# Performance work log

Hardware: AMD Instinct MI355X
Metric: run time of the kernel (lower is better)

Reference implementation:

```python
import jax, jax.numpy as jnp
import numpy as np

T, B, I, H = 2048, 512, 1, 64


def setup_inputs() -> dict:
    key = jax.random.key(0)
    ks = jax.random.split(key, 8)
    s_in = 1.0 / np.sqrt(H)  # torch RNN/Linear init scale (uniform bound)
    return {
        "x": jax.random.normal(ks[0], (T, B, I), dtype=jnp.float32),
        "h": jax.random.normal(ks[1], (1, B, H), dtype=jnp.float32),
        "W_ih": jax.random.uniform(ks[2], (H, I), jnp.float32, -s_in, s_in),
        "W_hh": jax.random.uniform(ks[3], (H, H), jnp.float32, -s_in, s_in),
        "b_ih": jax.random.uniform(ks[4], (H,), jnp.float32, -s_in, s_in),
        "b_hh": jax.random.uniform(ks[5], (H,), jnp.float32, -s_in, s_in),
        "W_lin": jax.random.uniform(ks[6], (1, H), jnp.float32, -s_in, s_in),
        "b_lin": jax.random.uniform(ks[7], (1,), jnp.float32, -s_in, s_in),
    }


def reference(x, h, W_ih, W_hh, b_ih, b_hh, W_lin, b_lin):
    # tanh RNN: h_t = tanh(x_t W_ih^T + b_ih + h_{t-1} W_hh^T + b_hh)
    h0 = h[0]  # [B, H]
    # precompute input projection for all timesteps: [T, B, H]
    xp = jnp.einsum('tbi,hi->tbh', x, W_ih) + b_ih + b_hh

    def step(h_prev, xp_t):
        h_new = jnp.tanh(xp_t + h_prev @ W_hh.T)
        return h_new, h_new

    h_last, hs = jax.lax.scan(step, h0, xp)  # hs: [T, B, H]
    y = jnp.einsum('tbh,oh->tbo', hs, W_lin) + b_lin  # [T, B, 1]
    return y, h_last[None]  # h_n: [1, B, H]
```

## Files before the change

kernel.cpp:

```cpp
#include <hip/hip_runtime.h>

#define TT 2048
#define BB 512
#define HH 64
#define NW 4
#define NTH (NW * 64)
#define HIST 128
#define HPAD 68

typedef float f32x2 __attribute__((ext_vector_type(2)));
typedef float f32x4 __attribute__((ext_vector_type(4)));

#define DPP_ADD(v, ctrl) \
    ((v) + __int_as_float(__builtin_amdgcn_update_dpp(0, __float_as_int(v), (ctrl), 0xF, 0xF, false)))

__global__ __launch_bounds__(NTH, 1) void rnn_fused(
    const float* __restrict__ x,
    const float* __restrict__ h0,
    const float* __restrict__ Wih,
    const float* __restrict__ Whh,
    const float* __restrict__ bih,
    const float* __restrict__ bhh,
    const float* __restrict__ Wlin,
    const float* __restrict__ blin,
    float* __restrict__ y,
    float* __restrict__ hN)
{
    __shared__ __align__(16) float hist[HIST][HPAD];
    __shared__ float xsh[TT + 4];
    __shared__ __align__(16) float wlin_sh[HH];

    const int b    = blockIdx.x;
    const int tid  = threadIdx.x;
    const int lane = tid & 63;
    const int w    = tid >> 6;
    const int hl   = lane >> 2;
    const int ks   = lane & 3;
    const int h    = w * 16 + hl;

    for (int i = tid; i < TT; i += NTH)
        xsh[i] = x[(size_t)i * BB + b];
    if (tid < 4) xsh[TT + tid] = 0.f;

    f32x2 wr[8];
    const float* wp = Whh + h * HH + ks * 16;
#pragma unroll
    for (int i = 0; i < 8; ++i) {
        wr[i][0] = wp[2 * i + 0];
        wr[i][1] = wp[2 * i + 1];
    }
    const float wih  = Wih[h];
    const float bias = bih[h] + bhh[h];
    const float bl   = blin[0];

    if (tid < HH) {
        hist[HIST - 1][tid] = h0[b * HH + tid];
        wlin_sh[tid] = Wlin[tid];
    }
    __syncthreads();

    float hval = 0.f;
    float xw = fmaf(xsh[0], wih, bias);

#pragma unroll 1
    for (int tc = 0; tc < TT; tc += HIST) {
#pragma unroll 2
        for (int ti = 0; ti < HIST; ++ti) {
            const int t  = tc + ti;
            const int rs = (ti + HIST - 1) & (HIST - 1);

            const f32x4* hp = reinterpret_cast<const f32x4*>(&hist[rs][ks * 16]);
            const f32x4 q0 = hp[0], q1 = hp[1], q2 = hp[2], q3 = hp[3];

            f32x2 a01 = {0.f, 0.f}, a23 = {0.f, 0.f};
            f32x2 a45 = {0.f, 0.f}, a67 = {0.f, 0.f};
            a01 = __builtin_elementwise_fma(__builtin_shufflevector(q0, q0, 0, 1), wr[0], a01);
            a23 = __builtin_elementwise_fma(__builtin_shufflevector(q0, q0, 2, 3), wr[1], a23);
            a45 = __builtin_elementwise_fma(__builtin_shufflevector(q1, q1, 0, 1), wr[2], a45);
            a67 = __builtin_elementwise_fma(__builtin_shufflevector(q1, q1, 2, 3), wr[3], a67);
            a01 = __builtin_elementwise_fma(__builtin_shufflevector(q2, q2, 0, 1), wr[4], a01);
            a23 = __builtin_elementwise_fma(__builtin_shufflevector(q2, q2, 2, 3), wr[5], a23);
            a45 = __builtin_elementwise_fma(__builtin_shufflevector(q3, q3, 0, 1), wr[6], a45);
            a67 = __builtin_elementwise_fma(__builtin_shufflevector(q3, q3, 2, 3), wr[7], a67);
            const f32x2 s2 = (a01 + a23) + (a45 + a67);
            float s = s2[0] + s2[1];

            s = DPP_ADD(s, 0xB1);
            s = DPP_ADD(s, 0x4E);

            const float acc = xw + s;

            const float e2 = __builtin_amdgcn_exp2f(acc * 2.885390081777927f);
            const float r  = __builtin_amdgcn_rcpf(e2 + 1.0f);
            hval = fmaf(-2.0f, r, 1.0f);

            if (ks == 0) hist[ti][h] = hval;

            xw = fmaf(xsh[t + 1], wih, bias);

            __syncthreads();
        }

        if (tid < HIST) {
            const f32x4* hp = reinterpret_cast<const f32x4*>(&hist[tid][0]);
            const f32x4* wl = reinterpret_cast<const f32x4*>(&wlin_sh[0]);
            f32x2 acc2 = {0.f, 0.f};
#pragma unroll
            for (int i = 0; i < 16; ++i) {
                const f32x4 q  = hp[i];
                const f32x4 qw = wl[i];
                acc2 = __builtin_elementwise_fma(__builtin_shufflevector(q, q, 0, 1),
                                                 __builtin_shufflevector(qw, qw, 0, 1), acc2);
                acc2 = __builtin_elementwise_fma(__builtin_shufflevector(q, q, 2, 3),
                                                 __builtin_shufflevector(qw, qw, 2, 3), acc2);
            }
            y[(size_t)(tc + tid) * BB + b] = acc2[0] + acc2[1] + bl;
        }
        __syncthreads();
    }

    if (ks == 0) hN[b * HH + h] = hval;
}

extern "C" void kernel_launch(void* const* d_in, const int* in_sizes, int n_in,
                              void* d_out, int out_size, void* d_ws, size_t ws_size,
                              hipStream_t stream) {
    const float* x    = (const float*)d_in[0];
    const float* h0   = (const float*)d_in[1];
    const float* Wih  = (const float*)d_in[2];
    const float* Whh  = (const float*)d_in[3];
    const float* bih  = (const float*)d_in[4];
    const float* bhh  = (const float*)d_in[5];
    const float* Wlin = (const float*)d_in[6];
    const float* blin = (const float*)d_in[7];

    float* y  = (float*)d_out;
    float* hN = (float*)d_out + TT * BB;

    rnn_fused<<<dim3(BB), dim3(NTH), 0, stream>>>(x, h0, Wih, Whh, bih, bhh, Wlin, blin, y, hN);
}
```

Before: 425.3 us.

## Use one wavefront per batch row with full-row dot, dropping block barriers

Each block now runs a single 64-lane wavefront. Every lane owns one hidden unit and computes the full 64-element dot product from 64 register-held weights, so the 4-way split with its DPP reduction and the per-timestep __syncthreads go away. The cost is four times more FMAs and LDS reads per lane on the serial critical path. Correctness without barriers depends on wavefront lockstep ordering of LDS writes and reads, which is fragile.

```diff
diff --git a/kernel.cpp b/kernel.cpp
--- a/kernel.cpp
+++ b/kernel.cpp
@@ -3,18 +3,17 @@
 #define TT 2048
 #define BB 512
 #define HH 64
-#define NW 4
-#define NTH (NW * 64)
 #define HIST 128
 #define HPAD 68
 
 typedef float f32x2 __attribute__((ext_vector_type(2)));
 typedef float f32x4 __attribute__((ext_vector_type(4)));
 
-#define DPP_ADD(v, ctrl) \
-    ((v) + __int_as_float(__builtin_amdgcn_update_dpp(0, __float_as_int(v), (ctrl), 0xF, 0xF, false)))
+#define FMA2(a, b, c) __builtin_elementwise_fma((a), (b), (c))
+#define LO2(q) __builtin_shufflevector((q), (q), 0, 1)
+#define HI2(q) __builtin_shufflevector((q), (q), 2, 3)
 
-__global__ __launch_bounds__(NTH, 1) void rnn_fused(
+__global__ __launch_bounds__(64, 1) void rnn_fused(
     const float* __restrict__ x,
     const float* __restrict__ h0,
     const float* __restrict__ Wih,
@@ -30,22 +29,17 @@
     __shared__ float xsh[TT + 4];
     __shared__ __align__(16) float wlin_sh[HH];
 
-    const int b    = blockIdx.x;
-    const int tid  = threadIdx.x;
-    const int lane = tid & 63;
-    const int w    = tid >> 6;
-    const int hl   = lane >> 2;
-    const int ks   = lane & 3;
-    const int h    = w * 16 + hl;
+    const int b = blockIdx.x;
+    const int h = threadIdx.x;
 
-    for (int i = tid; i < TT; i += NTH)
+    for (int i = h; i < TT; i += 64)
         xsh[i] = x[(size_t)i * BB + b];
-    if (tid < 4) xsh[TT + tid] = 0.f;
+    if (h < 4) xsh[TT + h] = 0.f;
 
-    f32x2 wr[8];
-    const float* wp = Whh + h * HH + ks * 16;
+    f32x2 wr[32];
+    const float* wp = Whh + h * HH;
 #pragma unroll
-    for (int i = 0; i < 8; ++i) {
+    for (int i = 0; i < 32; ++i) {
         wr[i][0] = wp[2 * i + 0];
         wr[i][1] = wp[2 * i + 1];
     }
@@ -53,73 +47,68 @@
     const float bias = bih[h] + bhh[h];
     const float bl   = blin[0];
 
-    if (tid < HH) {
-        hist[HIST - 1][tid] = h0[b * HH + tid];
-        wlin_sh[tid] = Wlin[tid];
-    }
-    __syncthreads();
+    wlin_sh[h] = Wlin[h];
+    hist[HIST - 1][h] = h0[b * HH + h];
 
     float hval = 0.f;
     float xw = fmaf(xsh[0], wih, bias);
 
 #pragma unroll 1
     for (int tc = 0; tc < TT; tc += HIST) {
-#pragma unroll 2
+#pragma unroll 4
         for (int ti = 0; ti < HIST; ++ti) {
             const int t  = tc + ti;
             const int rs = (ti + HIST - 1) & (HIST - 1);
 
-            const f32x4* hp = reinterpret_cast<const f32x4*>(&hist[rs][ks * 16]);
-            const f32x4 q0 = hp[0], q1 = hp[1], q2 = hp[2], q3 = hp[3];
+            const f32x4* hp = reinterpret_cast<const f32x4*>(&hist[rs][0]);
 
-            f32x2 a01 = {0.f, 0.f}, a23 = {0.f, 0.f};
+            f32x2 a01 = {xw, 0.f}, a23 = {0.f, 0.f};
             f32x2 a45 = {0.f, 0.f}, a67 = {0.f, 0.f};
-            a01 = __builtin_elementwise_fma(__builtin_shufflevector(q0, q0, 0, 1), wr[0], a01);
-            a23 = __builtin_elementwise_fma(__builtin_shufflevector(q0, q0, 2, 3), wr[1], a23);
-            a45 = __builtin_elementwise_fma(__builtin_shufflevector(q1, q1, 0, 1), wr[2], a45);
-            a67 = __builtin_elementwise_fma(__builtin_shufflevector(q1, q1, 2, 3), wr[3], a67);
-            a01 = __builtin_elementwise_fma(__builtin_shufflevector(q2, q2, 0, 1), wr[4], a01);
-            a23 = __builtin_elementwise_fma(__builtin_shufflevector(q2, q2, 2, 3), wr[5], a23);
-            a45 = __builtin_elementwise_fma(__builtin_shufflevector(q3, q3, 0, 1), wr[6], a45);
-            a67 = __builtin_elementwise_fma(__builtin_shufflevector(q3, q3, 2, 3), wr[7], a67);
+#pragma unroll
+            for (int j = 0; j < 4; ++j) {
+                const f32x4 p0 = hp[4 * j + 0];
+                const f32x4 p1 = hp[4 * j + 1];
+                const f32x4 p2 = hp[4 * j + 2];
+                const f32x4 p3 = hp[4 * j + 3];
+                a01 = FMA2(LO2(p0), wr[8 * j + 0], a01);
+                a23 = FMA2(HI2(p0), wr[8 * j + 1], a23);
+                a45 = FMA2(LO2(p1), wr[8 * j + 2], a45);
+                a67 = FMA2(HI2(p1), wr[8 * j + 3], a67);
+                a01 = FMA2(LO2(p2), wr[8 * j + 4], a01);
+                a23 = FMA2(HI2(p2), wr[8 * j + 5], a23);
+                a45 = FMA2(LO2(p3), wr[8 * j + 6], a45);
+                a67 = FMA2(HI2(p3), wr[8 * j + 7], a67);
+            }
             const f32x2 s2 = (a01 + a23) + (a45 + a67);
-            float s = s2[0] + s2[1];
-
-            s = DPP_ADD(s, 0xB1);
-            s = DPP_ADD(s, 0x4E);
-
-            const float acc = xw + s;
+            const float acc = s2[0] + s2[1];
 
             const float e2 = __builtin_amdgcn_exp2f(acc * 2.885390081777927f);
             const float r  = __builtin_amdgcn_rcpf(e2 + 1.0f);
             hval = fmaf(-2.0f, r, 1.0f);
 
-            if (ks == 0) hist[ti][h] = hval;
+            hist[ti][h] = hval;
 
             xw = fmaf(xsh[t + 1], wih, bias);
-
-            __syncthreads();
         }
 
-        if (tid < HIST) {
-            const f32x4* hp = reinterpret_cast<const f32x4*>(&hist[tid][0]);
+#pragma unroll 1
+        for (int rep = 0; rep < 2; ++rep) {
+            const int slot = rep * 64 + h;
+            const f32x4* rp = reinterpret_cast<const f32x4*>(&hist[slot][0]);
             const f32x4* wl = reinterpret_cast<const f32x4*>(&wlin_sh[0]);
             f32x2 acc2 = {0.f, 0.f};
 #pragma unroll
             for (int i = 0; i < 16; ++i) {
-                const f32x4 q  = hp[i];
+                const f32x4 q  = rp[i];
                 const f32x4 qw = wl[i];
-                acc2 = __builtin_elementwise_fma(__builtin_shufflevector(q, q, 0, 1),
-                                                 __builtin_shufflevector(qw, qw, 0, 1), acc2);
-                acc2 = __builtin_elementwise_fma(__builtin_shufflevector(q, q, 2, 3),
-                                                 __builtin_shufflevector(qw, qw, 2, 3), acc2);
+                acc2 = FMA2(LO2(q), LO2(qw), acc2);
+                acc2 = FMA2(HI2(q), HI2(qw), acc2);
             }
-            y[(size_t)(tc + tid) * BB + b] = acc2[0] + acc2[1] + bl;
+            y[(size_t)(tc + slot) * BB + b] = acc2[0] + acc2[1] + bl;
         }
-        __syncthreads();
     }
 
-    if (ks == 0) hN[b * HH + h] = hval;
+    hN[b * HH + h] = hval;
 }
 
 extern "C" void kernel_launch(void* const* d_in, const int* in_sizes, int n_in,
@@ -137,5 +126,5 @@
     float* y  = (float*)d_out;
     float* hN = (float*)d_out + TT * BB;
 
-    rnn_fused<<<dim3(BB), dim3(NTH), 0, stream>>>(x, h0, Wih, Whh, bih, bhh, Wlin, blin, y, hN);
+    rnn_fused<<<dim3(BB), dim3(64), 0, stream>>>(x, h0, Wih, Whh, bih, bhh, Wlin, blin, y, hN);
 }
```

Result: faster. 347.1 us (-18.4%).
